# Optimization experiments

Hardware: AMD Instinct MI355X
Metric: run time of the kernel (lower is better)

## Reference

```python
import jax, jax.numpy as jnp
import numpy as np

N, T, IN = 20000, 30, 32
H = 64          # lstm hidden
HEADS = 4
OUT = 32
E = 320000
NEG_SLOPE = 0.2


def _lstm_layer(x, Wih, Whh, bih, bhh):
    # x: [N, T, in]; Wih: [in, 4H]; Whh: [H, 4H]
    n, t, _ = x.shape
    h_dim = Whh.shape[0]
    xW = x @ Wih + bih  # [N, T, 4H]
    xW = jnp.transpose(xW, (1, 0, 2))  # [T, N, 4H]

    def step(carry, xt):
        h, c = carry
        g = xt + h @ Whh + bhh
        i, f, gg, o = jnp.split(g, 4, axis=-1)  # torch gate order i,f,g,o
        i = jax.nn.sigmoid(i)
        f = jax.nn.sigmoid(f)
        gg = jnp.tanh(gg)
        o = jax.nn.sigmoid(o)
        c = f * c + i * gg
        h = o * jnp.tanh(c)
        return (h, c), h

    init = (jnp.zeros((n, h_dim), x.dtype), jnp.zeros((n, h_dim), x.dtype))
    _, hs = jax.lax.scan(step, init, xW)
    return jnp.transpose(hs, (1, 0, 2))  # [N, T, H]


def _gat(x, edge_index, W, att_src, att_dst, bias, n):
    # x: [N, F_in]; W: [F_in, heads*C]; att_*: [heads, C]
    heads, C = att_src.shape
    h = (x @ W).reshape(n, heads, C)
    src, dst = edge_index[0], edge_index[1]
    a_src = jnp.einsum('nhc,hc->nh', h, att_src)  # [N, heads]
    a_dst = jnp.einsum('nhc,hc->nh', h, att_dst)
    logits = jax.nn.leaky_relu(a_src[src] + a_dst[dst], NEG_SLOPE)  # [E, heads]
    # segment softmax over destination nodes (every node has a self loop)
    m = jax.ops.segment_max(logits, dst, num_segments=n)
    e = jnp.exp(logits - m[dst])
    s = jax.ops.segment_sum(e, dst, num_segments=n)
    alpha = e / s[dst]
    out = jax.ops.segment_sum(alpha[:, :, None] * h[src], dst, num_segments=n)
    return out.reshape(n, heads * C) + bias


def setup_inputs() -> dict:
    key = jax.random.key(0)
    ks = jax.random.split(key, 20)
    sc = 0.05
    inp = {
        'x': jax.random.normal(ks[0], (N, T, IN), jnp.float32),
        'edge_index': jax.random.randint(ks[1], (2, E), 0, N, jnp.int64),
        # LSTM layer 0
        'Wih0': jax.random.normal(ks[2], (IN, 4 * H), jnp.float32) * sc,
        'Whh0': jax.random.normal(ks[3], (H, 4 * H), jnp.float32) * sc,
        'bih0': jnp.zeros((4 * H,), jnp.float32),
        'bhh0': jnp.zeros((4 * H,), jnp.float32),
        # LSTM layer 1
        'Wih1': jax.random.normal(ks[4], (H, 4 * H), jnp.float32) * sc,
        'Whh1': jax.random.normal(ks[5], (H, 4 * H), jnp.float32) * sc,
        'bih1': jnp.zeros((4 * H,), jnp.float32),
        'bhh1': jnp.zeros((4 * H,), jnp.float32),
        # GAT layer 1: H -> H per head, HEADS heads, concat
        'W1': jax.random.normal(ks[6], (H, HEADS * H), jnp.float32) * sc,
        'as1': jax.random.normal(ks[7], (HEADS, H), jnp.float32) * sc,
        'ad1': jax.random.normal(ks[8], (HEADS, H), jnp.float32) * sc,
        'b1': jnp.zeros((HEADS * H,), jnp.float32),
        # GAT layer 2: HEADS*H -> OUT, 1 head
        'W2': jax.random.normal(ks[9], (HEADS * H, OUT), jnp.float32) * sc,
        'as2': jax.random.normal(ks[10], (1, OUT), jnp.float32) * sc,
        'ad2': jax.random.normal(ks[11], (1, OUT), jnp.float32) * sc,
        'b2': jnp.zeros((OUT,), jnp.float32),
    }
    return inp


def reference(x, edge_index, Wih0, Whh0, bih0, bhh0, Wih1, Whh1, bih1, bhh1,
              W1, as1, ad1, b1, W2, as2, ad2, b2):
    n = x.shape[0]
    # add self loops (PyG GATConv default add_self_loops=True)
    loops = jnp.arange(n, dtype=edge_index.dtype)
    ei = jnp.concatenate([edge_index, jnp.stack([loops, loops])], axis=1)
    # 2-layer LSTM, take last timestep hidden state per node
    h = _lstm_layer(x, Wih0, Whh0, bih0, bhh0)
    h = _lstm_layer(h, Wih1, Whh1, bih1, bhh1)
    h = h[:, -1, :]  # [N, H]
    h = _gat(h, ei, W1, as1, ad1, b1, n)
    h = jax.nn.relu(h)
    out = _gat(h, ei, W2, as2, ad2, b2, n)
    return out
```

## Files before the change

kernel.cpp:

```cpp
#include <hip/hip_runtime.h>
#include <math.h>

#define Tt  30
#define INP 32
#define HID 64
#define NEG 0.2f
#define P   72

typedef __attribute__((ext_vector_type(8))) _Float16 half8;
typedef __attribute__((ext_vector_type(4))) float    f4;

#define MFMA16(a,b,c) __builtin_amdgcn_mfma_f32_16x16x32_f16((a),(b),(c),0,0,0)

__device__ __forceinline__ float fsigm(float v){ return __builtin_amdgcn_rcpf(1.f + __expf(-v)); }
__device__ __forceinline__ float ftanh(float v){ return 2.f * __builtin_amdgcn_rcpf(1.f + __expf(-2.f*v)) - 1.f; }

__device__ __forceinline__ float f16lo(unsigned u){
    union{unsigned short s; _Float16 f;} c; c.s = (unsigned short)(u & 0xffffu); return (float)c.f;
}
__device__ __forceinline__ float f16hi(unsigned u){
    union{unsigned short s; _Float16 f;} c; c.s = (unsigned short)(u >> 16); return (float)c.f;
}

__device__ __forceinline__ void loadW(const float* __restrict__ Wa, const float* __restrict__ Wb,
                                      int R0, int kt, int quad, int col, half8& H){
    #pragma unroll
    for (int e = 0; e < 8; ++e){
        int r = kt*32 + quad*8 + e;
        float v = (r < R0) ? Wa[r*256 + col] : Wb[(r - R0)*256 + col];
        H[e] = (_Float16)v;
    }
}

__global__ __launch_bounds__(256, 2) void k_lstm_fused(
    const float* __restrict__ x,
    const float* __restrict__ Wih0, const float* __restrict__ Whh0,
    const float* __restrict__ bih0, const float* __restrict__ bhh0,
    const float* __restrict__ Wih1, const float* __restrict__ Whh1,
    const float* __restrict__ bih1, const float* __restrict__ bhh1,
    float* __restrict__ h1last)
{
    __shared__ _Float16 sH0[2][16 * P];
    __shared__ _Float16 sH1[2][16 * P];

    const int tid = threadIdx.x, lane = tid & 63, j = tid >> 6;
    const int quad = lane >> 4, ln = lane & 15;
    const int jc = j * 16 + ln;
    const int n0 = blockIdx.x * 16;

    half8 w0[3][4];
    #pragma unroll
    for (int kt = 0; kt < 3; ++kt)
        #pragma unroll
        for (int g = 0; g < 4; ++g)
            loadW(Wih0, Whh0, 32, kt, quad, g*64 + jc, w0[kt][g]);

    half8 w1[4][4];
    #pragma unroll
    for (int kt = 0; kt < 4; ++kt)
        #pragma unroll
        for (int g = 0; g < 4; ++g)
            loadW(Wih1, Whh1, 64, kt, quad, g*64 + jc, w1[kt][g]);

    float b0[4], b1v[4];
    #pragma unroll
    for (int g = 0; g < 4; ++g){
        b0[g]  = bih0[g*64 + jc] + bhh0[g*64 + jc];
        b1v[g] = bih1[g*64 + jc] + bhh1[g*64 + jc];
    }

    float c0[4] = {0.f,0.f,0.f,0.f};
    float c1[4] = {0.f,0.f,0.f,0.f};

    for (int idx = tid; idx < 16*P; idx += 256){
        sH0[0][idx] = (_Float16)0.f; sH1[0][idx] = (_Float16)0.f;
    }
    __syncthreads();

    const float* xrow = x + (size_t)(n0 + ln) * (Tt*INP) + quad*8;
    float4 nxa = *(const float4*)xrow, nxb = *(const float4*)(xrow + 4);

    #pragma unroll 1
    for (int t = 0; t < Tt; ++t){
        const int pb = t & 1;
        _Float16* h0r = sH0[pb];
        _Float16* h0w = sH0[pb ^ 1];
        _Float16* h1r = sH1[pb];
        _Float16* h1w = sH1[pb ^ 1];

        float4 xa = nxa, xb = nxb;
        if (t + 1 < Tt){
            nxa = *(const float4*)(xrow + (t+1)*INP);
            nxb = *(const float4*)(xrow + (t+1)*INP + 4);
        }
        half8 xf;
        xf[0]=(_Float16)xa.x; xf[1]=(_Float16)xa.y; xf[2]=(_Float16)xa.z; xf[3]=(_Float16)xa.w;
        xf[4]=(_Float16)xb.x; xf[5]=(_Float16)xb.y; xf[6]=(_Float16)xb.z; xf[7]=(_Float16)xb.w;

        half8 h0a = *(const half8*)(h0r + ln*P + quad*8);
        half8 h0b = *(const half8*)(h0r + ln*P + 32 + quad*8);
        {
            f4 acc[4];
            #pragma unroll
            for (int g = 0; g < 4; ++g){
                f4 a = {b0[g], b0[g], b0[g], b0[g]};
                a = MFMA16(xf,  w0[0][g], a);
                a = MFMA16(h0a, w0[1][g], a);
                a = MFMA16(h0b, w0[2][g], a);
                acc[g] = a;
            }
            #pragma unroll
            for (int r = 0; r < 4; ++r){
                float iv = fsigm(acc[0][r]), fv = fsigm(acc[1][r]);
                float gv = ftanh(acc[2][r]), ov = fsigm(acc[3][r]);
                c0[r] = fv * c0[r] + iv * gv;
                h0w[(quad*4 + r)*P + jc] = (_Float16)(ov * ftanh(c0[r]));
            }
        }
        __syncthreads();

        half8 a0 = *(const half8*)(h0w + ln*P + quad*8);
        half8 a1 = *(const half8*)(h0w + ln*P + 32 + quad*8);
        half8 a2 = *(const half8*)(h1r + ln*P + quad*8);
        half8 a3 = *(const half8*)(h1r + ln*P + 32 + quad*8);
        {
            f4 acc[4];
            #pragma unroll
            for (int g = 0; g < 4; ++g){
                f4 a = {b1v[g], b1v[g], b1v[g], b1v[g]};
                a = MFMA16(a0, w1[0][g], a);
                a = MFMA16(a1, w1[1][g], a);
                a = MFMA16(a2, w1[2][g], a);
                a = MFMA16(a3, w1[3][g], a);
                acc[g] = a;
            }
            #pragma unroll
            for (int r = 0; r < 4; ++r){
                float iv = fsigm(acc[0][r]), fv = fsigm(acc[1][r]);
                float gv = ftanh(acc[2][r]), ov = fsigm(acc[3][r]);
                c1[r] = fv * c1[r] + iv * gv;
                float hv = ov * ftanh(c1[r]);
                h1w[(quad*4 + r)*P + jc] = (_Float16)hv;
                if (t == Tt-1) h1last[(size_t)(n0 + quad*4 + r)*HID + jc] = hv;
            }
        }
    }
}

__global__ __launch_bounds__(256) void k_gproj1(
    const float* __restrict__ hl, const float* __restrict__ W1,
    const float* __restrict__ as1, const float* __restrict__ ad1,
    _Float16* __restrict__ H1, float* __restrict__ a_s, float* __restrict__ a_d)
{
    __shared__ float sh[16][64];
    const int tid = threadIdx.x;
    const int n0 = blockIdx.x * 16;
    for (int idx = tid; idx < 16*64; idx += 256)
        sh[idx >> 6][idx & 63] = hl[(size_t)(n0 + (idx >> 6)) * 64 + (idx & 63)];
    __syncthreads();
    float acc[16];
    #pragma unroll
    for (int r = 0; r < 16; ++r) acc[r] = 0.f;
    for (int j = 0; j < 64; ++j){
        float w = W1[j * 256 + tid];
        #pragma unroll
        for (int r = 0; r < 16; ++r) acc[r] += sh[r][j] * w;
    }
    const float asv = as1[tid], adv = ad1[tid];
    const int wv = tid >> 6;
    #pragma unroll
    for (int r = 0; r < 16; ++r){
        H1[(size_t)(n0 + r) * 256 + tid] = (_Float16)acc[r];
        float ls = acc[r] * asv, ld = acc[r] * adv;
        #pragma unroll
        for (int off = 32; off >= 1; off >>= 1){ ls += __shfl_down(ls, off); ld += __shfl_down(ld, off); }
        if ((tid & 63) == 0){ a_s[(n0 + r) * 4 + wv] = ls; a_d[(n0 + r) * 4 + wv] = ld; }
    }
}

__global__ __launch_bounds__(256) void k_gproj2(
    const _Float16* __restrict__ h2, const float* __restrict__ W2,
    const float* __restrict__ as2, const float* __restrict__ ad2,
    _Float16* __restrict__ H2, float* __restrict__ a2s, float* __restrict__ a2d)
{
    __shared__ float sh[16][260];
    const int tid = threadIdx.x;
    const int n0 = blockIdx.x * 16;
    for (int idx = tid; idx < 16*256; idx += 256)
        sh[idx >> 8][idx & 255] = (float)h2[(size_t)(n0 + (idx >> 8)) * 256 + (idx & 255)];
    __syncthreads();
    const int c = tid & 31, rg = tid >> 5;
    float a0 = 0.f, a1 = 0.f;
    for (int j = 0; j < 256; ++j){
        float w = W2[j * 32 + c];
        a0 += sh[rg*2][j] * w;
        a1 += sh[rg*2 + 1][j] * w;
    }
    const float asv = as2[c], adv = ad2[c];
    H2[(size_t)(n0 + rg*2) * 32 + c]     = (_Float16)a0;
    H2[(size_t)(n0 + rg*2 + 1) * 32 + c] = (_Float16)a1;
    float s0 = a0 * asv, d0 = a0 * adv, s1 = a1 * asv, d1 = a1 * adv;
    #pragma unroll
    for (int off = 16; off >= 1; off >>= 1){
        s0 += __shfl_down(s0, off, 32); d0 += __shfl_down(d0, off, 32);
        s1 += __shfl_down(s1, off, 32); d1 += __shfl_down(d1, off, 32);
    }
    if (c == 0){
        a2s[n0 + rg*2] = s0;     a2d[n0 + rg*2] = d0;
        a2s[n0 + rg*2 + 1] = s1; a2d[n0 + rg*2 + 1] = d1;
    }
}

__global__ void k_count(const int* __restrict__ ei, int* __restrict__ deg, int E, int Et)
{
    int e = blockIdx.x * blockDim.x + threadIdx.x;
    if (e >= Et) return;
    int d = (e < E) ? ei[E + e] : e - E;
    atomicAdd(&deg[d], 1);
}

__global__ __launch_bounds__(256) void k_scanA(const int* __restrict__ deg, int* __restrict__ off,
                                               int* __restrict__ csum, int N)
{
    __shared__ int sm[256];
    int b = blockIdx.x, tid = threadIdx.x, i = b * 256 + tid;
    int v = (i < N) ? deg[i] : 0;
    sm[tid] = v;
    __syncthreads();
    #pragma unroll
    for (int s = 1; s < 256; s <<= 1) {
        int t = (tid >= s) ? sm[tid - s] : 0;
        __syncthreads();
        sm[tid] += t;
        __syncthreads();
    }
    if (i < N) off[i] = sm[tid] - v;
    if (tid == 255) csum[b] = sm[255];
}

__global__ __launch_bounds__(256) void k_scanB(int* __restrict__ csum, int NC)
{
    __shared__ int sm[256];
    const int tid = threadIdx.x;
    if (NC > 256){
        if (tid == 0){ int run = 0; for (int b = 0; b < NC; ++b){ int t = csum[b]; csum[b] = run; run += t; } }
        return;
    }
    int v = (tid < NC) ? csum[tid] : 0;
    sm[tid] = v;
    __syncthreads();
    #pragma unroll
    for (int s = 1; s < 256; s <<= 1){
        int t = (tid >= s) ? sm[tid - s] : 0;
        __syncthreads();
        sm[tid] += t;
        __syncthreads();
    }
    if (tid < NC) csum[tid] = sm[tid] - v;
}

__global__ __launch_bounds__(256) void k_scanC(int* __restrict__ off, const int* __restrict__ csum,
                                               int* __restrict__ cursor, int N)
{
    int i = blockIdx.x * blockDim.x + threadIdx.x;
    if (i < N){ int v = off[i] + csum[i >> 8]; off[i] = v; cursor[i] = v; }
}

__global__ void k_fill(const int* __restrict__ ei, int* __restrict__ cursor,
                       int* __restrict__ elist, int E, int Et)
{
    int e = blockIdx.x * blockDim.x + threadIdx.x;
    if (e >= Et) return;
    int s, d;
    if (e < E) { s = ei[e]; d = ei[E + e]; } else { s = d = e - E; }
    int slot = atomicAdd(&cursor[d], 1);
    elist[slot] = s;
}

__global__ __launch_bounds__(256) void k_gat1(
    const int* __restrict__ off, const int* __restrict__ deg, const int* __restrict__ elist,
    const float* __restrict__ a_s, const float* __restrict__ a_d,
    const _Float16* __restrict__ H1, const float* __restrict__ b1,
    _Float16* __restrict__ h2, int N)
{
    const int d = blockIdx.x * 4 + (threadIdx.x >> 6);
    if (d >= N) return;
    const int lane = threadIdx.x & 63;
    const int h = lane >> 4;
    const int base = off[d], n_e = deg[d];
    const float add = a_d[d * 4 + h];
    const uint2* H1v = (const uint2*)H1;

    float acc0 = 0.f, acc1 = 0.f, acc2 = 0.f, acc3 = 0.f, asum = 0.f;
    int e = 0;
    for (; e + 4 <= n_e; e += 4) {
        int s0 = elist[base + e],     s1 = elist[base + e + 1];
        int s2 = elist[base + e + 2], s3 = elist[base + e + 3];
        float A0 = a_s[s0 * 4 + h] + add, A1 = a_s[s1 * 4 + h] + add;
        float A2 = a_s[s2 * 4 + h] + add, A3 = a_s[s3 * 4 + h] + add;
        uint2 u0 = H1v[(size_t)s0 * 64 + lane], u1 = H1v[(size_t)s1 * 64 + lane];
        uint2 u2 = H1v[(size_t)s2 * 64 + lane], u3 = H1v[(size_t)s3 * 64 + lane];
        float l0 = A0 > 0.f ? A0 : NEG * A0, l1 = A1 > 0.f ? A1 : NEG * A1;
        float l2 = A2 > 0.f ? A2 : NEG * A2, l3 = A3 > 0.f ? A3 : NEG * A3;
        float al0 = __expf(l0), al1 = __expf(l1), al2 = __expf(l2), al3 = __expf(l3);
        acc0 += al0*f16lo(u0.x) + al1*f16lo(u1.x) + al2*f16lo(u2.x) + al3*f16lo(u3.x);
        acc1 += al0*f16hi(u0.x) + al1*f16hi(u1.x) + al2*f16hi(u2.x) + al3*f16hi(u3.x);
        acc2 += al0*f16lo(u0.y) + al1*f16lo(u1.y) + al2*f16lo(u2.y) + al3*f16lo(u3.y);
        acc3 += al0*f16hi(u0.y) + al1*f16hi(u1.y) + al2*f16hi(u2.y) + al3*f16hi(u3.y);
        asum += al0 + al1 + al2 + al3;
    }
    for (; e < n_e; ++e) {
        int s0 = elist[base + e];
        float A0 = a_s[s0 * 4 + h] + add;
        uint2 u0 = H1v[(size_t)s0 * 64 + lane];
        float l0 = A0 > 0.f ? A0 : NEG * A0;
        float al0 = __expf(l0);
        acc0 += al0 * f16lo(u0.x); acc1 += al0 * f16hi(u0.x);
        acc2 += al0 * f16lo(u0.y); acc3 += al0 * f16hi(u0.y);
        asum += al0;
    }
    const float r = __builtin_amdgcn_rcpf(asum);
    const float4 bv = *(const float4*)(b1 + lane * 4);
    float v0 = acc0 * r + bv.x, v1 = acc1 * r + bv.y;
    float v2 = acc2 * r + bv.z, v3 = acc3 * r + bv.w;
    v0 = v0 > 0.f ? v0 : 0.f; v1 = v1 > 0.f ? v1 : 0.f;
    v2 = v2 > 0.f ? v2 : 0.f; v3 = v3 > 0.f ? v3 : 0.f;
    union { uint2 u; _Float16 f[4]; } pk;
    pk.f[0] = (_Float16)v0; pk.f[1] = (_Float16)v1;
    pk.f[2] = (_Float16)v2; pk.f[3] = (_Float16)v3;
    ((uint2*)h2)[(size_t)d * 64 + lane] = pk.u;
}

__global__ __launch_bounds__(256) void k_gat2(
    const int* __restrict__ off, const int* __restrict__ deg, const int* __restrict__ elist,
    const float* __restrict__ a2s, const float* __restrict__ a2d,
    const _Float16* __restrict__ H2, const float* __restrict__ b2,
    float* __restrict__ outp)
{
    const int d = blockIdx.x * 4 + (threadIdx.x >> 6);
    const int lane = threadIdx.x & 63;
    const int base = off[d], n_e = deg[d];
    const float add = a2d[d];
    const int half = lane >> 5, c = lane & 31;

    float acc = 0.f, asum = 0.f;
    int e = half;
    for (; e + 2 < n_e; e += 4) {
        int s0 = elist[base + e], s1 = elist[base + e + 2];
        float a0 = a2s[s0] + add, a1 = a2s[s1] + add;
        float l0 = a0 > 0.f ? a0 : NEG * a0, l1 = a1 > 0.f ? a1 : NEG * a1;
        float al0 = __expf(l0), al1 = __expf(l1);
        acc  += al0 * (float)H2[(size_t)s0 * 32 + c];
        acc  += al1 * (float)H2[(size_t)s1 * 32 + c];
        asum += al0 + al1;
    }
    if (e < n_e) {
        int s0 = elist[base + e];
        float a0 = a2s[s0] + add;
        float l0 = a0 > 0.f ? a0 : NEG * a0;
        float al0 = __expf(l0);
        acc  += al0 * (float)H2[(size_t)s0 * 32 + c];
        asum += al0;
    }
    acc  += __shfl_down(acc, 32);
    asum += __shfl_down(asum, 32);
    if (lane < 32) outp[(size_t)d * 32 + c] = acc * __builtin_amdgcn_rcpf(asum) + b2[c];
}

static inline int cdiv(long long a, long long b) { return (int)((a + b - 1) / b); }

extern "C" void kernel_launch(void* const* d_in, const int* in_sizes, int n_in,
                              void* d_out, int out_size, void* d_ws, size_t ws_size,
                              hipStream_t stream)
{
    const float* x    = (const float*)d_in[0];
    const int*   ei   = (const int*)d_in[1];
    const float* Wih0 = (const float*)d_in[2];
    const float* Whh0 = (const float*)d_in[3];
    const float* bih0 = (const float*)d_in[4];
    const float* bhh0 = (const float*)d_in[5];
    const float* Wih1 = (const float*)d_in[6];
    const float* Whh1 = (const float*)d_in[7];
    const float* bih1 = (const float*)d_in[8];
    const float* bhh1 = (const float*)d_in[9];
    const float* W1   = (const float*)d_in[10];
    const float* as1  = (const float*)d_in[11];
    const float* ad1  = (const float*)d_in[12];
    const float* b1   = (const float*)d_in[13];
    const float* W2   = (const float*)d_in[14];
    const float* as2  = (const float*)d_in[15];
    const float* ad2  = (const float*)d_in[16];
    const float* b2   = (const float*)d_in[17];
    float* outp = (float*)d_out;

    const int N  = in_sizes[0] / (Tt * INP);
    const int E  = in_sizes[1] / 2;
    const int Et = E + N;
    const int NC = cdiv(N, 256);

    float* ws = (float*)d_ws;
    float* h1last = ws;
    _Float16* H1 = (_Float16*)(h1last + (size_t)N * 64);
    _Float16* h2 = (_Float16*)((float*)H1 + (size_t)N * 256);
    _Float16* H2 = (_Float16*)((float*)h2 + (size_t)N * 256);
    float* as1p = (float*)H2 + (size_t)N * 32;
    float* ad1p = as1p + (size_t)N * 4;
    float* a2s  = ad1p + (size_t)N * 4;
    float* a2d  = a2s + N;
    int* deg    = (int*)(a2d + N);
    int* off    = deg + N;
    int* cursor = off + N;
    int* csum   = cursor + N;
    int* elist  = csum + NC;

    k_lstm_fused<<<dim3(N / 16), dim3(256), 0, stream>>>(
        x, Wih0, Whh0, bih0, bhh0, Wih1, Whh1, bih1, bhh1, h1last);

    hipMemsetAsync(deg, 0, (size_t)N * 4, stream);
    k_count<<<cdiv(Et, 256), 256, 0, stream>>>(ei, deg, E, Et);
    k_scanA<<<NC, 256, 0, stream>>>(deg, off, csum, N);
    k_scanB<<<1, 256, 0, stream>>>(csum, NC);
    k_scanC<<<NC, 256, 0, stream>>>(off, csum, cursor, N);
    k_fill<<<cdiv(Et, 256), 256, 0, stream>>>(ei, cursor, elist, E, Et);

    k_gproj1<<<dim3(N / 16), dim3(256), 0, stream>>>(h1last, W1, as1, ad1, H1, as1p, ad1p);
    k_gat1<<<dim3(cdiv(N, 4)), dim3(256), 0, stream>>>(off, deg, elist, as1p, ad1p, H1, b1, h2, N);

    k_gproj2<<<dim3(N / 16), dim3(256), 0, stream>>>(h2, W2, as2, ad2, H2, a2s, a2d);
    k_gat2<<<dim3(N / 4), dim3(256), 0, stream>>>(off, deg, elist, a2s, a2d, H2, b2, outp);
}
```

Baseline: 374.2 us.

## Fuse GAT1 projection into LSTM kernel and GAT2 projection into GAT1 aggregation

Computes the first GAT projection (x@W1 plus attention logits) at the end of the LSTM kernel, reading the final hidden state from shared memory, so the fp32 h1last round-trip and the k_gproj1 launch go away. The layer-1 aggregation kernel now handles 16 destination nodes per block, keeps the ReLU output in shared memory and applies the W2 projection there, removing the h2 buffer and the k_gproj2 launch. The trade-offs are longer tails on the LSTM kernel, less parallelism in the aggregation (a quarter as many blocks, each looping over 4 sub-batches) and a shared-memory increase that may lower occupancy.

Measured after the change: 365.3 us. -2.4%, faster.

```diff
diff --git a/kernel.cpp b/kernel.cpp
--- a/kernel.cpp
+++ b/kernel.cpp
@@ -38,7 +38,9 @@
     const float* __restrict__ bih0, const float* __restrict__ bhh0,
     const float* __restrict__ Wih1, const float* __restrict__ Whh1,
     const float* __restrict__ bih1, const float* __restrict__ bhh1,
-    float* __restrict__ h1last)
+    const float* __restrict__ W1,  const float* __restrict__ as1,
+    const float* __restrict__ ad1,
+    _Float16* __restrict__ H1, float* __restrict__ a_s, float* __restrict__ a_d)
 {
     __shared__ _Float16 sH0[2][16 * P];
     __shared__ _Float16 sH1[2][16 * P];
@@ -139,75 +141,35 @@
                 float iv = fsigm(acc[0][r]), fv = fsigm(acc[1][r]);
                 float gv = ftanh(acc[2][r]), ov = fsigm(acc[3][r]);
                 c1[r] = fv * c1[r] + iv * gv;
-                float hv = ov * ftanh(c1[r]);
-                h1w[(quad*4 + r)*P + jc] = (_Float16)hv;
-                if (t == Tt-1) h1last[(size_t)(n0 + quad*4 + r)*HID + jc] = hv;
+                h1w[(quad*4 + r)*P + jc] = (_Float16)(ov * ftanh(c1[r]));
             }
         }
     }
-}
-
-__global__ __launch_bounds__(256) void k_gproj1(
-    const float* __restrict__ hl, const float* __restrict__ W1,
-    const float* __restrict__ as1, const float* __restrict__ ad1,
-    _Float16* __restrict__ H1, float* __restrict__ a_s, float* __restrict__ a_d)
-{
-    __shared__ float sh[16][64];
-    const int tid = threadIdx.x;
-    const int n0 = blockIdx.x * 16;
-    for (int idx = tid; idx < 16*64; idx += 256)
-        sh[idx >> 6][idx & 63] = hl[(size_t)(n0 + (idx >> 6)) * 64 + (idx & 63)];
+
     __syncthreads();
-    float acc[16];
-    #pragma unroll
-    for (int r = 0; r < 16; ++r) acc[r] = 0.f;
-    for (int j = 0; j < 64; ++j){
-        float w = W1[j * 256 + tid];
+    const unsigned* h1u = (const unsigned*)sH1[0];
+    {
+        float acc[16];
         #pragma unroll
-        for (int r = 0; r < 16; ++r) acc[r] += sh[r][j] * w;
-    }
-    const float asv = as1[tid], adv = ad1[tid];
-    const int wv = tid >> 6;
-    #pragma unroll
-    for (int r = 0; r < 16; ++r){
-        H1[(size_t)(n0 + r) * 256 + tid] = (_Float16)acc[r];
-        float ls = acc[r] * asv, ld = acc[r] * adv;
+        for (int r = 0; r < 16; ++r) acc[r] = 0.f;
+        for (int jj = 0; jj < 64; jj += 2){
+            float wA = W1[jj * 256 + tid];
+            float wB = W1[(jj + 1) * 256 + tid];
+            #pragma unroll
+            for (int r = 0; r < 16; ++r){
+                unsigned u = h1u[(r * P + jj) >> 1];
+                acc[r] += f16lo(u) * wA + f16hi(u) * wB;
+            }
+        }
+        const float asv = as1[tid], adv = ad1[tid];
         #pragma unroll
-        for (int off = 32; off >= 1; off >>= 1){ ls += __shfl_down(ls, off); ld += __shfl_down(ld, off); }
-        if ((tid & 63) == 0){ a_s[(n0 + r) * 4 + wv] = ls; a_d[(n0 + r) * 4 + wv] = ld; }
-    }
-}
-
-__global__ __launch_bounds__(256) void k_gproj2(
-    const _Float16* __restrict__ h2, const float* __restrict__ W2,
-    const float* __restrict__ as2, const float* __restrict__ ad2,
-    _Float16* __restrict__ H2, float* __restrict__ a2s, float* __restrict__ a2d)
-{
-    __shared__ float sh[16][260];
-    const int tid = threadIdx.x;
-    const int n0 = blockIdx.x * 16;
-    for (int idx = tid; idx < 16*256; idx += 256)
-        sh[idx >> 8][idx & 255] = (float)h2[(size_t)(n0 + (idx >> 8)) * 256 + (idx & 255)];
-    __syncthreads();
-    const int c = tid & 31, rg = tid >> 5;
-    float a0 = 0.f, a1 = 0.f;
-    for (int j = 0; j < 256; ++j){
-        float w = W2[j * 32 + c];
-        a0 += sh[rg*2][j] * w;
-        a1 += sh[rg*2 + 1][j] * w;
-    }
-    const float asv = as2[c], adv = ad2[c];
-    H2[(size_t)(n0 + rg*2) * 32 + c]     = (_Float16)a0;
-    H2[(size_t)(n0 + rg*2 + 1) * 32 + c] = (_Float16)a1;
-    float s0 = a0 * asv, d0 = a0 * adv, s1 = a1 * asv, d1 = a1 * adv;
-    #pragma unroll
-    for (int off = 16; off >= 1; off >>= 1){
-        s0 += __shfl_down(s0, off, 32); d0 += __shfl_down(d0, off, 32);
-        s1 += __shfl_down(s1, off, 32); d1 += __shfl_down(d1, off, 32);
-    }
-    if (c == 0){
-        a2s[n0 + rg*2] = s0;     a2d[n0 + rg*2] = d0;
-        a2s[n0 + rg*2 + 1] = s1; a2d[n0 + rg*2 + 1] = d1;
+        for (int r = 0; r < 16; ++r){
+            H1[(size_t)(n0 + r) * 256 + tid] = (_Float16)acc[r];
+            float ls = acc[r] * asv, ld = acc[r] * adv;
+            #pragma unroll
+            for (int off = 32; off >= 1; off >>= 1){ ls += __shfl_down(ls, off); ld += __shfl_down(ld, off); }
+            if (lane == 0){ a_s[(n0 + r) * 4 + j] = ls; a_d[(n0 + r) * 4 + j] = ld; }
+        }
     }
 }
 
@@ -277,58 +239,85 @@
     elist[slot] = s;
 }
 
-__global__ __launch_bounds__(256) void k_gat1(
+__global__ __launch_bounds__(256) void k_gat1p2(
     const int* __restrict__ off, const int* __restrict__ deg, const int* __restrict__ elist,
     const float* __restrict__ a_s, const float* __restrict__ a_d,
     const _Float16* __restrict__ H1, const float* __restrict__ b1,
-    _Float16* __restrict__ h2, int N)
-{
-    const int d = blockIdx.x * 4 + (threadIdx.x >> 6);
-    if (d >= N) return;
-    const int lane = threadIdx.x & 63;
+    const float* __restrict__ W2, const float* __restrict__ as2, const float* __restrict__ ad2,
+    _Float16* __restrict__ H2, float* __restrict__ a2s, float* __restrict__ a2d)
+{
+    __shared__ float sh2[16][264];
+    const int tid = threadIdx.x;
+    const int n0 = blockIdx.x * 16;
+    const int w = tid >> 6, lane = tid & 63;
     const int h = lane >> 4;
-    const int base = off[d], n_e = deg[d];
-    const float add = a_d[d * 4 + h];
     const uint2* H1v = (const uint2*)H1;
-
-    float acc0 = 0.f, acc1 = 0.f, acc2 = 0.f, acc3 = 0.f, asum = 0.f;
-    int e = 0;
-    for (; e + 4 <= n_e; e += 4) {
-        int s0 = elist[base + e],     s1 = elist[base + e + 1];
-        int s2 = elist[base + e + 2], s3 = elist[base + e + 3];
-        float A0 = a_s[s0 * 4 + h] + add, A1 = a_s[s1 * 4 + h] + add;
-        float A2 = a_s[s2 * 4 + h] + add, A3 = a_s[s3 * 4 + h] + add;
-        uint2 u0 = H1v[(size_t)s0 * 64 + lane], u1 = H1v[(size_t)s1 * 64 + lane];
-        uint2 u2 = H1v[(size_t)s2 * 64 + lane], u3 = H1v[(size_t)s3 * 64 + lane];
-        float l0 = A0 > 0.f ? A0 : NEG * A0, l1 = A1 > 0.f ? A1 : NEG * A1;
-        float l2 = A2 > 0.f ? A2 : NEG * A2, l3 = A3 > 0.f ? A3 : NEG * A3;
-        float al0 = __expf(l0), al1 = __expf(l1), al2 = __expf(l2), al3 = __expf(l3);
-        acc0 += al0*f16lo(u0.x) + al1*f16lo(u1.x) + al2*f16lo(u2.x) + al3*f16lo(u3.x);
-        acc1 += al0*f16hi(u0.x) + al1*f16hi(u1.x) + al2*f16hi(u2.x) + al3*f16hi(u3.x);
-        acc2 += al0*f16lo(u0.y) + al1*f16lo(u1.y) + al2*f16lo(u2.y) + al3*f16lo(u3.y);
-        acc3 += al0*f16hi(u0.y) + al1*f16hi(u1.y) + al2*f16hi(u2.y) + al3*f16hi(u3.y);
-        asum += al0 + al1 + al2 + al3;
-    }
-    for (; e < n_e; ++e) {
-        int s0 = elist[base + e];
-        float A0 = a_s[s0 * 4 + h] + add;
-        uint2 u0 = H1v[(size_t)s0 * 64 + lane];
-        float l0 = A0 > 0.f ? A0 : NEG * A0;
-        float al0 = __expf(l0);
-        acc0 += al0 * f16lo(u0.x); acc1 += al0 * f16hi(u0.x);
-        acc2 += al0 * f16lo(u0.y); acc3 += al0 * f16hi(u0.y);
-        asum += al0;
-    }
-    const float r = __builtin_amdgcn_rcpf(asum);
     const float4 bv = *(const float4*)(b1 + lane * 4);
-    float v0 = acc0 * r + bv.x, v1 = acc1 * r + bv.y;
-    float v2 = acc2 * r + bv.z, v3 = acc3 * r + bv.w;
-    v0 = v0 > 0.f ? v0 : 0.f; v1 = v1 > 0.f ? v1 : 0.f;
-    v2 = v2 > 0.f ? v2 : 0.f; v3 = v3 > 0.f ? v3 : 0.f;
-    union { uint2 u; _Float16 f[4]; } pk;
-    pk.f[0] = (_Float16)v0; pk.f[1] = (_Float16)v1;
-    pk.f[2] = (_Float16)v2; pk.f[3] = (_Float16)v3;
-    ((uint2*)h2)[(size_t)d * 64 + lane] = pk.u;
+
+    #pragma unroll 1
+    for (int sub = 0; sub < 4; ++sub){
+        const int d = n0 + sub * 4 + w;
+        const int base = off[d], n_e = deg[d];
+        const float add = a_d[d * 4 + h];
+
+        float acc0 = 0.f, acc1 = 0.f, acc2 = 0.f, acc3 = 0.f, asum = 0.f;
+        int e = 0;
+        for (; e + 4 <= n_e; e += 4) {
+            int s0 = elist[base + e],     s1 = elist[base + e + 1];
+            int s2 = elist[base + e + 2], s3 = elist[base + e + 3];
+            float A0 = a_s[s0 * 4 + h] + add, A1 = a_s[s1 * 4 + h] + add;
+            float A2 = a_s[s2 * 4 + h] + add, A3 = a_s[s3 * 4 + h] + add;
+            uint2 u0 = H1v[(size_t)s0 * 64 + lane], u1 = H1v[(size_t)s1 * 64 + lane];
+            uint2 u2 = H1v[(size_t)s2 * 64 + lane], u3 = H1v[(size_t)s3 * 64 + lane];
+            float l0 = A0 > 0.f ? A0 : NEG * A0, l1 = A1 > 0.f ? A1 : NEG * A1;
+            float l2 = A2 > 0.f ? A2 : NEG * A2, l3 = A3 > 0.f ? A3 : NEG * A3;
+            float al0 = __expf(l0), al1 = __expf(l1), al2 = __expf(l2), al3 = __expf(l3);
+            acc0 += al0*f16lo(u0.x) + al1*f16lo(u1.x) + al2*f16lo(u2.x) + al3*f16lo(u3.x);
+            acc1 += al0*f16hi(u0.x) + al1*f16hi(u1.x) + al2*f16hi(u2.x) + al3*f16hi(u3.x);
+            acc2 += al0*f16lo(u0.y) + al1*f16lo(u1.y) + al2*f16lo(u2.y) + al3*f16lo(u3.y);
+            acc3 += al0*f16hi(u0.y) + al1*f16hi(u1.y) + al2*f16hi(u2.y) + al3*f16hi(u3.y);
+            asum += al0 + al1 + al2 + al3;
+        }
+        for (; e < n_e; ++e) {
+            int s0 = elist[base + e];
+            float A0 = a_s[s0 * 4 + h] + add;
+            uint2 u0 = H1v[(size_t)s0 * 64 + lane];
+            float l0 = A0 > 0.f ? A0 : NEG * A0;
+            float al0 = __expf(l0);
+            acc0 += al0 * f16lo(u0.x); acc1 += al0 * f16hi(u0.x);
+            acc2 += al0 * f16lo(u0.y); acc3 += al0 * f16hi(u0.y);
+            asum += al0;
+        }
+        const float r = __builtin_amdgcn_rcpf(asum);
+        float v0 = acc0 * r + bv.x, v1 = acc1 * r + bv.y;
+        float v2 = acc2 * r + bv.z, v3 = acc3 * r + bv.w;
+        v0 = v0 > 0.f ? v0 : 0.f; v1 = v1 > 0.f ? v1 : 0.f;
+        v2 = v2 > 0.f ? v2 : 0.f; v3 = v3 > 0.f ? v3 : 0.f;
+        float4 row = {v0, v1, v2, v3};
+        *(float4*)(&sh2[sub * 4 + w][lane * 4]) = row;
+    }
+    __syncthreads();
+
+    const int c = tid & 31, rg = tid >> 5;
+    float a0 = 0.f, a1 = 0.f;
+    for (int jj = 0; jj < 256; ++jj){
+        float wv = W2[jj * 32 + c];
+        a0 += sh2[rg*2][jj] * wv;
+        a1 += sh2[rg*2 + 1][jj] * wv;
+    }
+    const float asv = as2[c], adv = ad2[c];
+    H2[(size_t)(n0 + rg*2) * 32 + c]     = (_Float16)a0;
+    H2[(size_t)(n0 + rg*2 + 1) * 32 + c] = (_Float16)a1;
+    float s0 = a0 * asv, d0 = a0 * adv, s1 = a1 * asv, d1 = a1 * adv;
+    #pragma unroll
+    for (int o = 16; o >= 1; o >>= 1){
+        s0 += __shfl_down(s0, o, 32); d0 += __shfl_down(d0, o, 32);
+        s1 += __shfl_down(s1, o, 32); d1 += __shfl_down(d1, o, 32);
+    }
+    if (c == 0){
+        a2s[n0 + rg*2] = s0;     a2d[n0 + rg*2] = d0;
+        a2s[n0 + rg*2 + 1] = s1; a2d[n0 + rg*2 + 1] = d1;
+    }
 }
 
 __global__ __launch_bounds__(256) void k_gat2(
@@ -399,11 +388,9 @@
     const int NC = cdiv(N, 256);
 
     float* ws = (float*)d_ws;
-    float* h1last = ws;
-    _Float16* H1 = (_Float16*)(h1last + (size_t)N * 64);
-    _Float16* h2 = (_Float16*)((float*)H1 + (size_t)N * 256);
-    _Float16* H2 = (_Float16*)((float*)h2 + (size_t)N * 256);
-    float* as1p = (float*)H2 + (size_t)N * 32;
+    _Float16* H1 = (_Float16*)ws;
+    _Float16* H2 = (_Float16*)(ws + (size_t)N * 128);
+    float* as1p = (float*)H2 + (size_t)N * 16;
     float* ad1p = as1p + (size_t)N * 4;
     float* a2s  = ad1p + (size_t)N * 4;
     float* a2d  = a2s + N;
@@ -414,7 +401,8 @@
     int* elist  = csum + NC;
 
     k_lstm_fused<<<dim3(N / 16), dim3(256), 0, stream>>>(
-        x, Wih0, Whh0, bih0, bhh0, Wih1, Whh1, bih1, bhh1, h1last);
+        x, Wih0, Whh0, bih0, bhh0, Wih1, Whh1, bih1, bhh1,
+        W1, as1, ad1, H1, as1p, ad1p);
 
     hipMemsetAsync(deg, 0, (size_t)N * 4, stream);
     k_count<<<cdiv(Et, 256), 256, 0, stream>>>(ei, deg, E, Et);
@@ -423,9 +411,8 @@
     k_scanC<<<NC, 256, 0, stream>>>(off, csum, cursor, N);
     k_fill<<<cdiv(Et, 256), 256, 0, stream>>>(ei, cursor, elist, E, Et);
 
-    k_gproj1<<<dim3(N / 16), dim3(256), 0, stream>>>(h1last, W1, as1, ad1, H1, as1p, ad1p);
-    k_gat1<<<dim3(cdiv(N, 4)), dim3(256), 0, stream>>>(off, deg, elist, as1p, ad1p, H1, b1, h2, N);
-
-    k_gproj2<<<dim3(N / 16), dim3(256), 0, stream>>>(h2, W2, as2, ad2, H2, a2s, a2d);
+    k_gat1p2<<<dim3(N / 16), dim3(256), 0, stream>>>(
+        off, deg, elist, as1p, ad1p, H1, b1, W2, as2, ad2, H2, a2s, a2d);
+
     k_gat2<<<dim3(N / 4), dim3(256), 0, stream>>>(off, deg, elist, a2s, a2d, H2, b2, outp);
 }
```
